# Kernel tuning notes

Hardware: AMD Instinct MI355X
Metric: run time of the kernel (lower is better)

## Reference

```python
import jax, jax.numpy as jnp
import numpy as np

WINDOW_SIZE = 11
SIGMA = 1.5
C1 = 0.01 ** 2
C2 = 0.03 ** 2


def _gaussian_window_3d(window_size=WINDOW_SIZE, sigma=SIGMA):
    # 1D gaussian, normalized, then separable outer product -> dense 3D kernel
    x = jnp.arange(window_size, dtype=jnp.float32)
    g = jnp.exp(-((x - window_size // 2) ** 2) / (2.0 * sigma ** 2))
    g = g / g.sum()
    w3 = g[:, None, None] * g[None, :, None] * g[None, None, :]  # [ws,ws,ws]
    return w3[None, None]  # [O=1, I=1, D, H, W]


def _conv3d_same(x, w):
    # x: [N,1,D,H,W], w: [1,1,ws,ws,ws]; 'SAME' padding matches torch padding=ws//2 for odd ws
    return jax.lax.conv_general_dilated(
        x, w, window_strides=(1, 1, 1), padding='SAME',
        dimension_numbers=('NCDHW', 'OIDHW', 'NCDHW'))


def setup_inputs() -> dict:
    key = jax.random.key(0)
    k1, k2 = jax.random.split(key)
    shape = (4, 1, 160, 160, 160)
    img1 = jax.random.uniform(k1, shape, dtype=jnp.float32)
    img2 = jax.random.uniform(k2, shape, dtype=jnp.float32)
    return {"img1": img1, "img2": img2}


def reference(img1, img2):
    window = _gaussian_window_3d()
    mu1 = _conv3d_same(img1, window)
    mu2 = _conv3d_same(img2, window)
    mu1_sq = mu1 * mu1
    mu2_sq = mu2 * mu2
    mu1_mu2 = mu1 * mu2
    sigma1_sq = _conv3d_same(img1 * img1, window) - mu1_sq
    sigma2_sq = _conv3d_same(img2 * img2, window) - mu2_sq
    sigma12 = _conv3d_same(img1 * img2, window) - mu1_mu2
    ssim_map = ((2.0 * mu1_mu2 + C1) * (2.0 * sigma12 + C2)) / (
        (mu1_sq + mu2_sq + C1) * (sigma1_sq + sigma2_sq + C2))
    return 1.0 - ssim_map.mean()
```

## Files before the change

### kernel.cpp

```cpp
#include <hip/hip_runtime.h>
#include <hip/hip_bf16.h>
#include <math.h>

#define WW     160
#define NBATCH 4
#define VOL    (160*160*160)
#define PLANE  (160*160)

#define C1f 0.0001f
#define C2f 0.0009f

#define RUN_H 32
#define NROWS (RUN_H + 10)
#define LDW   176
#define RUN_D 40

typedef float v2f __attribute__((ext_vector_type(2)));

struct Gw { float g[11]; };

__device__ __forceinline__ float bf2f(unsigned short u) {
    return __uint_as_float(((unsigned int)u) << 16);
}
__device__ __forceinline__ unsigned short f2bf(float f) {
    __hip_bfloat16 h = __float2bfloat16(f);
    return *reinterpret_cast<unsigned short*>(&h);
}

__global__ __launch_bounds__(192, 5) void k_wh(
    const float* __restrict__ x, const float* __restrict__ y,
    ushort4* __restrict__ B4, unsigned short* __restrict__ B1, Gw gw)
{
    __shared__ unsigned int tile[NROWS][LDW];
    const int t  = threadIdx.x;
    const int h0 = blockIdx.x * RUN_H;
    const int d  = blockIdx.y;
    const int n  = blockIdx.z;

    const float* xb = x + (size_t)n * VOL + (size_t)d * PLANE;
    const float* yb = y + (size_t)n * VOL + (size_t)d * PLANE;

#pragma unroll 4
    for (int s = t; s < NROWS * LDW; s += 192) {
        int r = s / LDW, c = s - r * LDW;
        int h = h0 - 5 + r;
        int w = c - 5;
        float vx = 0.f, vy = 0.f;
        if (h >= 0 && h < 160 && w >= 0 && w < 160) {
            size_t idx = (size_t)h * WW + w;
            vx = xb[idx];
            vy = yb[idx];
        }
        tile[r][c] = ((unsigned int)f2bf(vy) << 16) | (unsigned int)f2bf(vx);
    }
    __syncthreads();

    if (t < 160) {
        const int w = t;
        const size_t outbase = (size_t)n * VOL + (size_t)d * PLANE + w;
        v2f ring01[11], ring23[11];
        float ring4[11];
#pragma unroll
        for (int i = 0; i < NROWS; ++i) {
            v2f a01 = {0.f, 0.f}, a23 = {0.f, 0.f};
            float a4 = 0.f;
#pragma unroll
            for (int k = 0; k < 5; ++k) {
                unsigned int u1 = tile[i][w + k];
                unsigned int u2 = tile[i][w + 10 - k];
                v2f xy1 = { __uint_as_float(u1 << 16), __uint_as_float(u1 & 0xffff0000u) };
                v2f xy2 = { __uint_as_float(u2 << 16), __uint_as_float(u2 & 0xffff0000u) };
                float g  = gw.g[k];
                v2f g2 = {g, g};
                a01 += g2 * (xy1 + xy2);
                v2f sq = xy1 * xy1;
                sq += xy2 * xy2;
                a23 += g2 * sq;
                float p = xy1.x * xy1.y;
                p = fmaf(xy2.x, xy2.y, p);
                a4 += g * p;
            }
            {
                unsigned int u = tile[i][w + 5];
                v2f xy = { __uint_as_float(u << 16), __uint_as_float(u & 0xffff0000u) };
                float g  = gw.g[5];
                v2f g2 = {g, g};
                a01 += g2 * xy;
                a23 += g2 * (xy * xy);
                a4  += g * (xy.x * xy.y);
            }
            ring01[i%11] = a01; ring23[i%11] = a23; ring4[i%11] = a4;

            if (i >= 10) {
                const int j = i - 10;
                v2f o01 = {0.f, 0.f}, o23 = {0.f, 0.f};
                float o4 = 0.f;
#pragma unroll
                for (int k = 0; k < 11; ++k) {
                    float g = gw.g[k];
                    v2f g2 = {g, g};
                    o01 += g2 * ring01[(j + k) % 11];
                    o23 += g2 * ring23[(j + k) % 11];
                    o4  += g  * ring4 [(j + k) % 11];
                }
                size_t oi = outbase + (size_t)(h0 + j) * WW;
                ushort4 u4;
                u4.x = f2bf(o01.x); u4.y = f2bf(o01.y);
                u4.z = f2bf(o23.x); u4.w = f2bf(o23.y);
                B4[oi] = u4;
                B1[oi] = f2bf(o4);
            }
        }
    }
}

__global__ __launch_bounds__(256, 3) void k_dssim(
    const ushort4* __restrict__ B4, const unsigned short* __restrict__ B1,
    double* __restrict__ accum, Gw gw)
{
    const int tid = threadIdx.x;
    const int p   = blockIdx.x * 256 + tid;
    const int d0  = blockIdx.y * RUN_D;
    const int n   = blockIdx.z;
    const size_t base = (size_t)n * VOL + p;

    v2f ring01[11], ring23[11];
    float ring4[11];
    float lsum = 0.f;

    ushort4 c4 = make_ushort4(0,0,0,0);
    unsigned short c1 = 0;
    {
        if (d0 != 0) {
            size_t idx = base + (size_t)(d0 - 5) * PLANE;
            c4 = B4[idx]; c1 = B1[idx];
        }
    }

#pragma unroll
    for (int i = 0; i < RUN_D + 10; ++i) {
        ring01[i%11] = (v2f){ bf2f(c4.x), bf2f(c4.y) };
        ring23[i%11] = (v2f){ bf2f(c4.z), bf2f(c4.w) };
        ring4 [i%11] = bf2f(c1);

        if (i + 1 < RUN_D + 10) {
            const int dd = d0 - 5 + i + 1;
            bool okNext = true;
            if (i + 1 < 5)              okNext = (d0 != 0);
            if (i + 1 >= RUN_D + 5)     okNext = (d0 != 120);
            c4 = make_ushort4(0,0,0,0); c1 = 0;
            if (okNext) {
                size_t idx = base + (size_t)dd * PLANE;
                c4 = B4[idx]; c1 = B1[idx];
            }
        }

        if (i >= 10) {
            const int j = i - 10;
            v2f o01 = {0.f, 0.f}, o23 = {0.f, 0.f};
            float o4 = 0.f;
#pragma unroll
            for (int k = 0; k < 11; ++k) {
                float g = gw.g[k];
                v2f g2 = {g, g};
                o01 += g2 * ring01[(j + k) % 11];
                o23 += g2 * ring23[(j + k) % 11];
                o4  += g  * ring4 [(j + k) % 11];
            }
            float mu1 = o01.x, mu2 = o01.y;
            float e11 = o23.x, e22 = o23.y, e12 = o4;
            float m11 = mu1 * mu2;
            float num = (2.f * m11 + C1f) * (2.f * (e12 - m11) + C2f);
            float den = (mu1 * mu1 + mu2 * mu2 + C1f) *
                        ((e11 - mu1 * mu1) + (e22 - mu2 * mu2) + C2f);
            lsum += num / den;
        }
    }

    __shared__ float wsum[4];
    const int lane = tid & 63, wi = tid >> 6;
#pragma unroll
    for (int off = 32; off > 0; off >>= 1)
        lsum += __shfl_down(lsum, off, 64);
    if (lane == 0) wsum[wi] = lsum;
    __syncthreads();
    if (tid == 0)
        atomicAdd(accum, (double)(wsum[0] + wsum[1] + wsum[2] + wsum[3]));
}

__global__ void k_final(const double* __restrict__ accum, float* __restrict__ out)
{
    out[0] = (float)(1.0 - accum[0] / ((double)NBATCH * (double)VOL));
}

extern "C" void kernel_launch(void* const* d_in, const int* in_sizes, int n_in,
                              void* d_out, int out_size, void* d_ws, size_t ws_size,
                              hipStream_t stream)
{
    const float* img1 = (const float*)d_in[0];
    const float* img2 = (const float*)d_in[1];
    float* out = (float*)d_out;

    char* ws = (char*)d_ws;
    ushort4* B4 = (ushort4*)ws;
    unsigned short* B1 = (unsigned short*)(ws + (size_t)NBATCH * VOL * 8);
    double* accum = (double*)(ws + (size_t)NBATCH * VOL * 10);

    Gw gw;
    {
        double gd[11], s = 0.0;
        for (int i = 0; i < 11; ++i) {
            double t = (double)(i - 5);
            gd[i] = exp(-(t * t) / (2.0 * 1.5 * 1.5));
            s += gd[i];
        }
        for (int i = 0; i < 11; ++i) gw.g[i] = (float)(gd[i] / s);
    }

    hipMemsetAsync(accum, 0, sizeof(double), stream);

    k_wh   <<<dim3(160 / RUN_H, 160, NBATCH), 192, 0, stream>>>(img1, img2, B4, B1, gw);
    k_dssim<<<dim3(PLANE / 256, 160 / RUN_D, NBATCH), 256, 0, stream>>>(B4, B1, accum, gw);
    k_final<<<1, 1, 0, stream>>>(accum, out);
}
```

Measured before the change: 340.2 us.

## Deepen depth-pass prefetch to five planes and halve H/D run lengths

The depth-convolution kernel now keeps a five-deep register prefetch queue of upcoming planes instead of loading only one plane ahead, so more global loads are in flight per thread. RUN_H and RUN_D are halved to launch more blocks, and the occupancy hint for the SSIM kernel rises from 3 to 4 blocks per CU. The costs are extra halo recomputation and reloading from the shorter runs, plus higher register pressure from the prefetch buffers, which may cause spills under the tighter launch bound.

After: 305.8 us. 10.1% less time.

```diff
diff --git a/kernel.cpp b/kernel.cpp
--- a/kernel.cpp
+++ b/kernel.cpp
@@ -10,10 +10,11 @@
 #define C1f 0.0001f
 #define C2f 0.0009f
 
-#define RUN_H 32
+#define RUN_H 16
 #define NROWS (RUN_H + 10)
 #define LDW   176
-#define RUN_D 40
+#define RUN_D 20
+#define PF    5
 
 typedef float v2f __attribute__((ext_vector_type(2)));
 
@@ -114,7 +115,7 @@
     }
 }
 
-__global__ __launch_bounds__(256, 3) void k_dssim(
+__global__ __launch_bounds__(256, 4) void k_dssim(
     const ushort4* __restrict__ B4, const unsigned short* __restrict__ B1,
     double* __restrict__ accum, Gw gw)
 {
@@ -128,30 +129,40 @@
     float ring4[11];
     float lsum = 0.f;
 
-    ushort4 c4 = make_ushort4(0,0,0,0);
-    unsigned short c1 = 0;
+    ushort4 pf4[PF];
+    unsigned short pf1[PF];
     {
-        if (d0 != 0) {
-            size_t idx = base + (size_t)(d0 - 5) * PLANE;
-            c4 = B4[idx]; c1 = B1[idx];
+        const bool front_ok = (d0 != 0);
+#pragma unroll
+        for (int q = 0; q < PF; ++q) {
+            pf4[q] = make_ushort4(0,0,0,0);
+            pf1[q] = 0;
+            if (front_ok) {
+                size_t idx = base + (size_t)(d0 - 5 + q) * PLANE;
+                pf4[q] = B4[idx];
+                pf1[q] = B1[idx];
+            }
         }
     }
 
 #pragma unroll
     for (int i = 0; i < RUN_D + 10; ++i) {
+        ushort4 c4 = pf4[i % PF];
+        unsigned short c1 = pf1[i % PF];
         ring01[i%11] = (v2f){ bf2f(c4.x), bf2f(c4.y) };
         ring23[i%11] = (v2f){ bf2f(c4.z), bf2f(c4.w) };
         ring4 [i%11] = bf2f(c1);
 
-        if (i + 1 < RUN_D + 10) {
-            const int dd = d0 - 5 + i + 1;
-            bool okNext = true;
-            if (i + 1 < 5)              okNext = (d0 != 0);
-            if (i + 1 >= RUN_D + 5)     okNext = (d0 != 120);
-            c4 = make_ushort4(0,0,0,0); c1 = 0;
-            if (okNext) {
+        if (i + PF < RUN_D + 10) {
+            const int dd = d0 + i;
+            bool ok = true;
+            if (i >= RUN_D) ok = (d0 != 160 - RUN_D);
+            pf4[i % PF] = make_ushort4(0,0,0,0);
+            pf1[i % PF] = 0;
+            if (ok) {
                 size_t idx = base + (size_t)dd * PLANE;
-                c4 = B4[idx]; c1 = B1[idx];
+                pf4[i % PF] = B4[idx];
+                pf1[i % PF] = B1[idx];
             }
         }
 
```
